# Optimization experiments

Measured on AMD Instinct MI355X. Metric: run time of the kernel, lower is better.

The kernel has to match this reference:

```python
import jax, jax.numpy as jnp
import numpy as np

C = 64
C8 = C // 8
C16 = C // 16


def setup_inputs() -> dict:
    key = jax.random.key(0)
    ks = jax.random.split(key, 11)
    s = lambda fan_in: 1.0 / np.sqrt(fan_in)
    return {
        "x": jax.random.normal(ks[0], (4, C, 64, 64), dtype=jnp.float32),
        # 1x1 convs == per-pixel linear: weight [out, in], bias [out]
        "Wq": jax.random.uniform(ks[1], (C8, C), minval=-s(C), maxval=s(C)),
        "bq": jax.random.uniform(ks[2], (C8,), minval=-s(C), maxval=s(C)),
        "Wk": jax.random.uniform(ks[3], (C8, C), minval=-s(C), maxval=s(C)),
        "bk": jax.random.uniform(ks[4], (C8,), minval=-s(C), maxval=s(C)),
        "Wv": jax.random.uniform(ks[5], (C, C), minval=-s(C), maxval=s(C)),
        "bv": jax.random.uniform(ks[6], (C,), minval=-s(C), maxval=s(C)),
        "W1": jax.random.uniform(ks[7], (C16, C), minval=-s(C), maxval=s(C)),
        "b1": jax.random.uniform(ks[8], (C16,), minval=-s(C), maxval=s(C)),
        "W2": jax.random.uniform(ks[9], (C, C16), minval=-s(C16), maxval=s(C16)),
        "b2": jax.random.uniform(ks[10], (C,), minval=-s(C16), maxval=s(C16)),
    }


def reference(x, Wq, bq, Wk, bk, Wv, bv, W1, b1, W2, b2):
    b, c, h, w = x.shape
    n = h * w
    xf = x.reshape(b, c, n)                                   # [b,c,n]
    Q = jnp.einsum('qc,bcn->bnq', Wq, xf) + bq                # [b,n,c/8]
    K = jnp.einsum('kc,bcn->bkn', Wk, xf) + bk[None, :, None] # [b,c/8,n]
    V = jnp.einsum('vc,bcn->bvn', Wv, xf) + bv[None, :, None] # [b,c,n]
    scores = jnp.einsum('bnq,bqm->bnm', Q, K) / jnp.sqrt(jnp.float32(c))
    att = jax.nn.softmax(scores, axis=-1)                     # [b,n,n]
    # self_attention_map = V @ att^T
    sa = jnp.einsum('bvm,bnm->bvn', V, att).reshape(b, c, h, w)
    # SE-style channel gate
    avg = xf.mean(axis=2)                                     # [b,c]
    gate = jax.nn.sigmoid(jax.nn.relu(avg @ W1.T + b1) @ W2.T + b2)
    return sa * gate[:, :, None, None]
```

## Files before the change

### kernel.cpp

```cpp
#include <hip/hip_runtime.h>
#include <hip/hip_bf16.h>

typedef __attribute__((ext_vector_type(8))) short bf16x8;
typedef __attribute__((ext_vector_type(4))) float f32x4;
typedef __attribute__((ext_vector_type(4))) unsigned short u16x4;
typedef __attribute__((ext_vector_type(8))) unsigned short u16x8;

#define WS_QB 0
#define WS_KB 131072
#define WS_VB 262144
#define WS_AVG_U 1310720

__device__ __forceinline__ unsigned short bf_hi(float x) {
    __hip_bfloat16 h = __float2bfloat16(x);
    return *reinterpret_cast<unsigned short*>(&h);
}

__global__ __launch_bounds__(256) void proj_kernel(
    const float* __restrict__ x,
    const float* __restrict__ Wq, const float* __restrict__ bq,
    const float* __restrict__ Wk, const float* __restrict__ bk,
    const float* __restrict__ Wv, const float* __restrict__ bv,
    unsigned short* __restrict__ Qb, unsigned short* __restrict__ Kb,
    unsigned short* __restrict__ Vb, float* __restrict__ avg)
{
    __shared__ __align__(16) unsigned short Wls[16 * 72];

    const int tid = threadIdx.x;
    const int w = tid >> 6;
    const int l = tid & 63;
    const int g = l >> 4;
    const int l15 = l & 15;

    const int tile = blockIdx.x >> 8;
    const int pair = blockIdx.x & 255;
    const int b = pair >> 6;
    const int n0 = (pair & 63) << 6;
    const int n = n0 + w * 16 + l15;
    const float* xb = x + b * 262144;

    float xr[2][8];
#pragma unroll
    for (int kcb = 0; kcb < 2; ++kcb)
#pragma unroll
        for (int j = 0; j < 8; ++j)
            xr[kcb][j] = xb[(kcb * 32 + g * 8 + j) * 4096 + n];

#pragma unroll
    for (int i = 0; i < 4; ++i) {
        const int idx = i * 256 + tid;
        const int row = idx >> 6, col = idx & 63;
        float wv;
        if (tile == 0) wv = (row < 8) ? Wq[row * 64 + col] : Wk[(row - 8) * 64 + col];
        else           wv = Wv[((tile - 1) * 16 + row) * 64 + col];
        Wls[row * 72 + col] = bf_hi(wv);
    }
    __syncthreads();

    bf16x8 bfr[2];
#pragma unroll
    for (int kcb = 0; kcb < 2; ++kcb)
#pragma unroll
        for (int j = 0; j < 8; ++j)
            bfr[kcb][j] = (short)bf_hi(xr[kcb][j]);

    const bf16x8 a0 = *(const bf16x8*)&Wls[l15 * 72 + g * 8];
    const bf16x8 a1 = *(const bf16x8*)&Wls[l15 * 72 + 32 + g * 8];
    f32x4 acc;
#pragma unroll
    for (int r = 0; r < 4; ++r) acc[r] = 0.0f;
    acc = __builtin_amdgcn_mfma_f32_16x16x32_bf16(a0, bfr[0], acc, 0, 0, 0);
    acc = __builtin_amdgcn_mfma_f32_16x16x32_bf16(a1, bfr[1], acc, 0, 0, 0);

    if (tile == 0) {
        u16x4 ov;
        if (g < 2) {
#pragma unroll
            for (int r = 0; r < 4; ++r) ov[r] = bf_hi((acc[r] + bq[g * 4 + r]) * 0.125f);
            *(u16x4*)&Qb[(b * 4096 + n) * 8 + g * 4] = ov;
        } else {
#pragma unroll
            for (int r = 0; r < 4; ++r) ov[r] = bf_hi(acc[r] + bk[(g - 2) * 4 + r]);
            *(u16x4*)&Kb[(b * 4096 + n) * 8 + (g - 2) * 4] = ov;
        }
        const int c = tid >> 2;
        const float* xrow = xb + c * 4096 + n0 + ((tid & 3) << 4);
        float s = 0.0f;
#pragma unroll
        for (int k = 0; k < 4; ++k) {
            const float4 v = *(const float4*)&xrow[k * 4];
            s += (v.x + v.y) + (v.z + v.w);
        }
        s += __shfl_xor(s, 1);
        s += __shfl_xor(s, 2);
        if ((tid & 3) == 0) atomicAdd(&avg[b * 64 + c], s * (1.0f / 4096.0f));
    } else {
#pragma unroll
        for (int r = 0; r < 4; ++r) {
            const int v = (tile - 1) * 16 + g * 4 + r;
            Vb[(b * 64 + v) * 4096 + n] = bf_hi(acc[r] + bv[v]);
        }
    }
}

__global__ __launch_bounds__(256) void attn_kernel(
    const unsigned short* __restrict__ Qb, const unsigned short* __restrict__ Kb,
    const unsigned short* __restrict__ Vb, const float* __restrict__ avg,
    const float* __restrict__ W1, const float* __restrict__ b1,
    const float* __restrict__ W2, const float* __restrict__ b2,
    float* __restrict__ out)
{
    __shared__ __align__(16) unsigned short Vs[2][64][64];
    __shared__ __align__(16) unsigned short Ps[2][32][64];
    __shared__ float zls[32], gls[64], avgs[64];

    const int t = threadIdx.x;
    const int w = t >> 6;
    const int l = t & 63;
    const int g = l >> 4;
    const int l15 = l & 15;

    const int wg = (blockIdx.x & 7) * 64 + (blockIdx.x >> 3);
    const int b = wg >> 7;
    const int q0 = (wg & 127) << 5;

    if (t < 32) zls[t] = 0.0f;
    if (t < 64) avgs[t] = avg[b * 64 + t];

    bf16x8 zf = {};
    bf16x8 qf[2];
#pragma unroll
    for (int qt = 0; qt < 2; ++qt) {
        bf16x8 v = *(const bf16x8*)&Qb[(b * 4096 + q0 + qt * 16 + l15) * 8];
        qf[qt] = (g == 0) ? v : zf;
    }

    const int srow = t >> 2;
    const int scol = (t & 3) << 4;
    const int ssw = (srow & 7) << 3;
    const unsigned short* vsrc = &Vb[(b * 64 + srow) * 4096];
    const int mrow = w * 16 + l15;

    u16x8 va = *(const u16x8*)&vsrc[scol];
    u16x8 vb2 = *(const u16x8*)&vsrc[scol + 8];
    bf16x8 kreg;
    {
        bf16x8 kv = *(const bf16x8*)&Kb[(b * 4096 + mrow) * 8];
        kreg = (g == 0) ? kv : zf;
    }

    f32x4 acc[2];
#pragma unroll
    for (int qt = 0; qt < 2; ++qt)
#pragma unroll
        for (int r = 0; r < 4; ++r) acc[qt][r] = 0.0f;
    float zreg[2] = {0.f, 0.f};
    const int vsw = (l15 & 7) << 3;
    const int psw = (l15 & 7) << 3;

    __syncthreads();

    for (int i = 0; i < 64; ++i) {
        const int buf = i & 1;

        {
            unsigned short* dst = &Vs[buf][srow][0];
            *(u16x8*)&dst[scol ^ ssw] = va;
            *(u16x8*)&dst[(scol + 8) ^ ssw] = vb2;
        }
        const bf16x8 kf = kreg;

        const int inx = (i < 63) ? i + 1 : 63;
        va  = *(const u16x8*)&vsrc[inx * 64 + scol];
        vb2 = *(const u16x8*)&vsrc[inx * 64 + scol + 8];
        {
            bf16x8 kv = *(const bf16x8*)&Kb[(b * 4096 + inx * 64 + mrow) * 8];
            kreg = (g == 0) ? kv : zf;
        }

        f32x4 dz;
#pragma unroll
        for (int r = 0; r < 4; ++r) dz[r] = 0.0f;
#pragma unroll
        for (int qt = 0; qt < 2; ++qt) {
            f32x4 d = __builtin_amdgcn_mfma_f32_16x16x32_bf16(kf, qf[qt], dz, 0, 0, 0);
            float p[4];
#pragma unroll
            for (int r = 0; r < 4; ++r) p[r] = __expf(d[r]);
            zreg[qt] += (p[0] + p[1]) + (p[2] + p[3]);
            u16x4 pw;
#pragma unroll
            for (int r = 0; r < 4; ++r) pw[r] = bf_hi(p[r]);
            const int q = qt * 16 + l15;
            *(u16x4*)&Ps[buf][q][(w * 16 + g * 4) ^ ((q & 7) << 3)] = pw;
        }

        __syncthreads();

        {
            const unsigned short* vbuf = &Vs[buf][w * 16 + l15][0];
            __builtin_amdgcn_s_setprio(1);
#pragma unroll
            for (int kcb = 0; kcb < 2; ++kcb) {
                const int colA = kcb * 32 + g * 8;
                const bf16x8 af = *(const bf16x8*)&vbuf[colA ^ vsw];
#pragma unroll
                for (int qt = 0; qt < 2; ++qt) {
                    const bf16x8 bfr = *(const bf16x8*)&Ps[buf][qt * 16 + l15][colA ^ psw];
                    acc[qt] = __builtin_amdgcn_mfma_f32_16x16x32_bf16(af, bfr, acc[qt], 0, 0, 0);
                }
            }
            __builtin_amdgcn_s_setprio(0);
        }
    }

#pragma unroll
    for (int qt = 0; qt < 2; ++qt) {
        float z = zreg[qt];
        z += __shfl_xor(z, 16);
        z += __shfl_xor(z, 32);
        if (g == 0) atomicAdd(&zls[qt * 16 + l15], z);
    }
    if (t < 64) {
        float hreg[4];
#pragma unroll
        for (int j = 0; j < 4; ++j) {
            float hh = b1[j];
            for (int c = 0; c < 64; ++c) hh += W1[j * 64 + c] * avgs[c];
            hreg[j] = fmaxf(hh, 0.0f);
        }
        float gg = b2[t];
#pragma unroll
        for (int j = 0; j < 4; ++j) gg += W2[t * 4 + j] * hreg[j];
        gls[t] = 1.0f / (1.0f + __expf(-gg));
    }
    __syncthreads();

#pragma unroll
    for (int qt = 0; qt < 2; ++qt) {
        const int q = qt * 16 + l15;
        const float rz = 1.0f / zls[q];
#pragma unroll
        for (int r = 0; r < 4; ++r) {
            const int v = w * 16 + g * 4 + r;
            out[(b * 64 + v) * 4096 + q0 + q] = acc[qt][r] * rz * gls[v];
        }
    }
}

extern "C" void kernel_launch(void* const* d_in, const int* in_sizes, int n_in,
                              void* d_out, int out_size, void* d_ws, size_t ws_size,
                              hipStream_t stream) {
    const float* x  = (const float*)d_in[0];
    const float* Wq = (const float*)d_in[1];
    const float* bq = (const float*)d_in[2];
    const float* Wk = (const float*)d_in[3];
    const float* bk = (const float*)d_in[4];
    const float* Wv = (const float*)d_in[5];
    const float* bv = (const float*)d_in[6];
    const float* W1 = (const float*)d_in[7];
    const float* b1 = (const float*)d_in[8];
    const float* W2 = (const float*)d_in[9];
    const float* b2 = (const float*)d_in[10];

    unsigned short* wsu = (unsigned short*)d_ws;
    unsigned short* Qb = wsu + WS_QB;
    unsigned short* Kb = wsu + WS_KB;
    unsigned short* Vb = wsu + WS_VB;
    float* avg = (float*)(wsu + WS_AVG_U);
    float* out = (float*)d_out;

    hipMemsetAsync(avg, 0, 256 * sizeof(float), stream);
    proj_kernel<<<1280, 256, 0, stream>>>(x, Wq, bq, Wk, bk, Wv, bv, Qb, Kb, Vb, avg);
    attn_kernel<<<512, 256, 0, stream>>>(Qb, Kb, Vb, avg, W1, b1, W2, b2, out);
}
```

Before: 114.2 us.

## Split key range across waves to remove per-iteration block barriers

New measurement: 117.7 us. +3.0%, slower.

```diff
diff --git a/kernel.cpp b/kernel.cpp
--- a/kernel.cpp
+++ b/kernel.cpp
@@ -103,15 +103,15 @@
     }
 }
 
-__global__ __launch_bounds__(256) void attn_kernel(
+__global__ __launch_bounds__(256, 2) void attn_kernel(
     const unsigned short* __restrict__ Qb, const unsigned short* __restrict__ Kb,
     const unsigned short* __restrict__ Vb, const float* __restrict__ avg,
     const float* __restrict__ W1, const float* __restrict__ b1,
     const float* __restrict__ W2, const float* __restrict__ b2,
     float* __restrict__ out)
 {
-    __shared__ __align__(16) unsigned short Vs[2][64][64];
-    __shared__ __align__(16) unsigned short Ps[2][32][64];
+    __shared__ __align__(16) unsigned short Pls[4][2][32][40];
+    __shared__ float osum[4][64][33];
     __shared__ float zls[32], gls[64], avgs[64];
 
     const int t = threadIdx.x;
@@ -126,6 +126,7 @@
 
     if (t < 32) zls[t] = 0.0f;
     if (t < 64) avgs[t] = avg[b * 64 + t];
+    __syncthreads();
 
     bf16x8 zf = {};
     bf16x8 qf[2];
@@ -135,83 +136,75 @@
         qf[qt] = (g == 0) ? v : zf;
     }
 
-    const int srow = t >> 2;
-    const int scol = (t & 3) << 4;
-    const int ssw = (srow & 7) << 3;
-    const unsigned short* vsrc = &Vb[(b * 64 + srow) * 4096];
-    const int mrow = w * 16 + l15;
-
-    u16x8 va = *(const u16x8*)&vsrc[scol];
-    u16x8 vb2 = *(const u16x8*)&vsrc[scol + 8];
-    bf16x8 kreg;
-    {
-        bf16x8 kv = *(const bf16x8*)&Kb[(b * 4096 + mrow) * 8];
-        kreg = (g == 0) ? kv : zf;
-    }
-
-    f32x4 acc[2];
+    const unsigned short* kb = Kb + b * 4096 * 8;
+    const unsigned short* vbB = Vb + (b * 64) * 4096;
+
+    int m0 = w * 32;
+    bf16x8 kpa = zf, kpb = zf;
+    if (g == 0) {
+        kpa = *(const bf16x8*)&kb[(m0 + l15) * 8];
+        kpb = *(const bf16x8*)&kb[(m0 + 16 + l15) * 8];
+    }
+    bf16x8 vp[4];
+#pragma unroll
+    for (int vt = 0; vt < 4; ++vt)
+        vp[vt] = *(const bf16x8*)&vbB[(vt * 16 + l15) * 4096 + m0 + g * 8];
+
+    f32x4 acc[2][4];
 #pragma unroll
     for (int qt = 0; qt < 2; ++qt)
 #pragma unroll
-        for (int r = 0; r < 4; ++r) acc[qt][r] = 0.0f;
+        for (int vt = 0; vt < 4; ++vt)
+#pragma unroll
+            for (int r = 0; r < 4; ++r) acc[qt][vt][r] = 0.0f;
     float zreg[2] = {0.f, 0.f};
-    const int vsw = (l15 & 7) << 3;
-    const int psw = (l15 & 7) << 3;
-
-    __syncthreads();
-
-    for (int i = 0; i < 64; ++i) {
-        const int buf = i & 1;
-
-        {
-            unsigned short* dst = &Vs[buf][srow][0];
-            *(u16x8*)&dst[scol ^ ssw] = va;
-            *(u16x8*)&dst[(scol + 8) ^ ssw] = vb2;
-        }
-        const bf16x8 kf = kreg;
-
-        const int inx = (i < 63) ? i + 1 : 63;
-        va  = *(const u16x8*)&vsrc[inx * 64 + scol];
-        vb2 = *(const u16x8*)&vsrc[inx * 64 + scol + 8];
-        {
-            bf16x8 kv = *(const bf16x8*)&Kb[(b * 4096 + inx * 64 + mrow) * 8];
-            kreg = (g == 0) ? kv : zf;
-        }
-
+
+    for (int ci = 0; ci < 32; ++ci) {
+        const bf16x8 ka = kpa, kc = kpb;
+        bf16x8 vc[4];
+#pragma unroll
+        for (int vt = 0; vt < 4; ++vt) vc[vt] = vp[vt];
+
+        const int m0n = (ci < 31) ? (w + 4 * (ci + 1)) * 32 : m0;
+        if (g == 0) {
+            kpa = *(const bf16x8*)&kb[(m0n + l15) * 8];
+            kpb = *(const bf16x8*)&kb[(m0n + 16 + l15) * 8];
+        }
+#pragma unroll
+        for (int vt = 0; vt < 4; ++vt)
+            vp[vt] = *(const bf16x8*)&vbB[(vt * 16 + l15) * 4096 + m0n + g * 8];
+
+        unsigned short* Pw = &Pls[w][ci & 1][0][0];
         f32x4 dz;
 #pragma unroll
         for (int r = 0; r < 4; ++r) dz[r] = 0.0f;
 #pragma unroll
-        for (int qt = 0; qt < 2; ++qt) {
-            f32x4 d = __builtin_amdgcn_mfma_f32_16x16x32_bf16(kf, qf[qt], dz, 0, 0, 0);
-            float p[4];
-#pragma unroll
-            for (int r = 0; r < 4; ++r) p[r] = __expf(d[r]);
-            zreg[qt] += (p[0] + p[1]) + (p[2] + p[3]);
-            u16x4 pw;
-#pragma unroll
-            for (int r = 0; r < 4; ++r) pw[r] = bf_hi(p[r]);
-            const int q = qt * 16 + l15;
-            *(u16x4*)&Ps[buf][q][(w * 16 + g * 4) ^ ((q & 7) << 3)] = pw;
-        }
-
-        __syncthreads();
-
-        {
-            const unsigned short* vbuf = &Vs[buf][w * 16 + l15][0];
-            __builtin_amdgcn_s_setprio(1);
-#pragma unroll
-            for (int kcb = 0; kcb < 2; ++kcb) {
-                const int colA = kcb * 32 + g * 8;
-                const bf16x8 af = *(const bf16x8*)&vbuf[colA ^ vsw];
-#pragma unroll
-                for (int qt = 0; qt < 2; ++qt) {
-                    const bf16x8 bfr = *(const bf16x8*)&Ps[buf][qt * 16 + l15][colA ^ psw];
-                    acc[qt] = __builtin_amdgcn_mfma_f32_16x16x32_bf16(af, bfr, acc[qt], 0, 0, 0);
-                }
+        for (int mt = 0; mt < 2; ++mt) {
+            const bf16x8 kf = mt ? kc : ka;
+#pragma unroll
+            for (int qt = 0; qt < 2; ++qt) {
+                f32x4 d = __builtin_amdgcn_mfma_f32_16x16x32_bf16(kf, qf[qt], dz, 0, 0, 0);
+                float p[4];
+#pragma unroll
+                for (int r = 0; r < 4; ++r) p[r] = __expf(d[r]);
+                zreg[qt] += (p[0] + p[1]) + (p[2] + p[3]);
+                u16x4 pw;
+#pragma unroll
+                for (int r = 0; r < 4; ++r) pw[r] = bf_hi(p[r]);
+                *(u16x4*)&Pw[(qt * 16 + l15) * 40 + mt * 16 + g * 4] = pw;
             }
-            __builtin_amdgcn_s_setprio(0);
-        }
+        }
+        const bf16x8 bp0 = *(const bf16x8*)&Pw[l15 * 40 + g * 8];
+        const bf16x8 bp1 = *(const bf16x8*)&Pw[(16 + l15) * 40 + g * 8];
+
+        __builtin_amdgcn_s_setprio(1);
+#pragma unroll
+        for (int vt = 0; vt < 4; ++vt) {
+            acc[0][vt] = __builtin_amdgcn_mfma_f32_16x16x32_bf16(vc[vt], bp0, acc[0][vt], 0, 0, 0);
+            acc[1][vt] = __builtin_amdgcn_mfma_f32_16x16x32_bf16(vc[vt], bp1, acc[1][vt], 0, 0, 0);
+        }
+        __builtin_amdgcn_s_setprio(0);
+        m0 = m0n;
     }
 
 #pragma unroll
@@ -221,6 +214,15 @@
         z += __shfl_xor(z, 32);
         if (g == 0) atomicAdd(&zls[qt * 16 + l15], z);
     }
+
+#pragma unroll
+    for (int qt = 0; qt < 2; ++qt)
+#pragma unroll
+        for (int vt = 0; vt < 4; ++vt)
+#pragma unroll
+            for (int r = 0; r < 4; ++r)
+                osum[w][vt * 16 + g * 4 + r][qt * 16 + l15] = acc[qt][vt][r];
+
     if (t < 64) {
         float hreg[4];
 #pragma unroll
@@ -236,14 +238,17 @@
     }
     __syncthreads();
 
-#pragma unroll
-    for (int qt = 0; qt < 2; ++qt) {
-        const int q = qt * 16 + l15;
-        const float rz = 1.0f / zls[q];
-#pragma unroll
-        for (int r = 0; r < 4; ++r) {
-            const int v = w * 16 + g * 4 + r;
-            out[(b * 64 + v) * 4096 + q0 + q] = acc[qt][r] * rz * gls[v];
+    {
+        const int v = t >> 2;
+        const int qb4 = (t & 3) * 8;
+        const float gv = gls[v];
+        float* orow = out + (b * 64 + v) * 4096 + q0 + qb4;
+#pragma unroll
+        for (int j = 0; j < 8; ++j) {
+            const int q = qb4 + j;
+            const float s = (osum[0][v][q] + osum[1][v][q])
+                          + (osum[2][v][q] + osum[3][v][q]);
+            orow[j] = s * (1.0f / zls[q]) * gv;
         }
     }
 }
```
